# Optimization experiments

Hardware: AMD Instinct MI355X
Metric: run time of the kernel (lower is better)

The kernel has to match this reference:

```python
import jax, jax.numpy as jnp
import numpy as np
from jax import lax

N_SEEDS = 16
N_SAMPS = 32
IN_C = 3
HID = [32, 64, 64]
K = 3
H = W = 64
EPS = 1e-5


def _uniform(key, shape, bound):
    return jax.random.uniform(key, shape, jnp.float32, -bound, bound)


def setup_inputs() -> dict:
    key = jax.random.key(0)
    keys = jax.random.split(key, 32)
    inp = {"x": jax.random.normal(keys[0], (N_SEEDS, N_SAMPS, IN_C, H, W), jnp.float32)}
    c_in = IN_C
    ki = 1
    for li, c_out in enumerate(HID, start=1):
        fan_in = c_in * K * K
        # kaiming_uniform with a=sqrt(5): gain=sqrt(2/(1+5))=sqrt(1/3); bound=sqrt(3)*gain/sqrt(fan)=1/sqrt(fan)
        wb = 1.0 / np.sqrt(fan_in)
        inp[f"w{li}"] = _uniform(keys[ki], (N_SEEDS * c_out, c_in, K, K), wb); ki += 1
        inp[f"b{li}"] = _uniform(keys[ki], (N_SEEDS * c_out,), wb); ki += 1
        inp[f"g{li}"] = jnp.ones((N_SEEDS * c_out,), jnp.float32)
        inp[f"be{li}"] = jnp.zeros((N_SEEDS * c_out,), jnp.float32)
        c_in = c_out
    return inp


def _layer(h, w, b, g, be):
    # grouped conv: groups = N_SEEDS, OIHW weights, NCHW data, stride 1, pad 1
    h = lax.conv_general_dilated(
        h, w, window_strides=(1, 1), padding=((1, 1), (1, 1)),
        feature_group_count=N_SEEDS,
        dimension_numbers=("NCHW", "OIHW", "NCHW"))
    h = h + b[None, :, None, None]
    # BatchNorm2d, training mode: batch statistics over (N, H, W), biased variance
    mean = jnp.mean(h, axis=(0, 2, 3))
    var = jnp.var(h, axis=(0, 2, 3))
    h = (h - mean[None, :, None, None]) * (g / jnp.sqrt(var + EPS))[None, :, None, None] + be[None, :, None, None]
    return jax.nn.relu(h)


def reference(x, w1, b1, g1, be1, w2, b2, g2, be2, w3, b3, g3, be3):
    S, N, C, Hh, Ww = x.shape  # (n_seeds, n_samps, C, H, W)
    h = jnp.swapaxes(x, 0, 1).reshape(N, S * C, Hh, Ww)
    h = _layer(h, w1, b1, g1, be1)
    h = _layer(h, w2, b2, g2, be2)
    h = _layer(h, w3, b3, g3, be3)
    c_out = HID[-1]
    h = h.reshape(N, S, c_out, Hh, Ww)
    return jnp.swapaxes(h, 0, 1)  # (n_seeds, n_samps, C_out, H, W)
```

## Files before the change

### kernel.cpp

```cpp
#include <hip/hip_runtime.h>
#include <cstddef>
#include <cstdint>

typedef __attribute__((ext_vector_type(8))) _Float16 half8;
typedef __attribute__((ext_vector_type(4))) float f32x4;
typedef _Float16 half_t;

#define NS 16
#define NN 32
#define NPIX 4096

static const size_t OFF_H1 = 0;
static const size_t OFF_H2 = 134217728ull;
static const size_t OFF_WT1 = OFF_H2 + 268435456ull;
static const size_t OFF_WT2 = OFF_WT1 + 55296ull;
static const size_t OFF_WT3 = OFF_WT2 + 589824ull;
static const size_t OFF_SUMS = OFF_WT3 + 1179648ull;
static const size_t OFF_PRM = OFF_SUMS + 20480ull;

__global__ __launch_bounds__(256) void transform_k(
    const float* __restrict__ w1, const float* __restrict__ w2,
    const float* __restrict__ w3, float* __restrict__ wt1,
    half_t* __restrict__ wt2, half_t* __restrict__ wt3)
{
    int idx = blockIdx.x * 256 + threadIdx.x;
    if (idx < 13824) {
        int o = idx & 31, tap = (idx >> 5) % 9, ic = (idx / 288) % 3, s = idx / 864;
        wt1[idx] = w1[((s * 32 + o) * 3 + ic) * 9 + tap];
    } else if (idx < 13824 + 294912) {
        int t = idx - 13824;
        int ic = t & 31, oc = (t >> 5) & 63, tap = (t >> 11) % 9, s = t / 18432;
        wt2[t] = (half_t)w2[((s * 64 + oc) * 32 + ic) * 9 + tap];
    } else {
        int t = idx - (13824 + 294912);
        int ic = t & 63, oc = (t >> 6) & 63, tap = (t >> 12) % 9, s = t / 36864;
        wt3[t] = (half_t)w3[((s * 64 + oc) * 64 + ic) * 9 + tap];
    }
}

__global__ __launch_bounds__(256) void conv1_k(
    const float* __restrict__ x, const float* __restrict__ wt1,
    const float* __restrict__ b1, half_t* __restrict__ h1,
    float* __restrict__ sums1)
{
    __shared__ float smem[8512];
    float* xt = smem;
    float* bounce = smem;
    float* statsl = smem + 8448;
    const int tile = blockIdx.x, s = blockIdx.y, n = blockIdx.z;
    const int tx = tile & 3, ty = tile >> 2, tid = threadIdx.x;

    for (int i = tid; i < 972; i += 256) {
        int ic = i / 324, rem = i - ic * 324;
        int py = rem / 18, px = rem - py * 18;
        int gy = ty * 16 + py - 1, gx = tx * 16 + px - 1;
        float v = 0.f;
        if ((unsigned)gy < 64u && (unsigned)gx < 64u)
            v = x[(size_t)(((s * NN + n) * 3 + ic) * 64 + gy) * 64 + gx];
        xt[i] = v;
    }
    if (tid < 64) statsl[tid] = 0.f;
    __syncthreads();

    const int px = tid & 15, py = tid >> 4;
    float acc[32];
#pragma unroll
    for (int o = 0; o < 32; ++o) acc[o] = 0.f;
#pragma unroll
    for (int ic = 0; ic < 3; ++ic)
#pragma unroll
        for (int ky = 0; ky < 3; ++ky)
#pragma unroll
            for (int kx = 0; kx < 3; ++kx) {
                float v = xt[ic * 324 + (py + ky) * 18 + px + kx];
                const float* wp = wt1 + ((s * 3 + ic) * 9 + ky * 3 + kx) * 32;
#pragma unroll
                for (int o = 0; o < 32; ++o) acc[o] = fmaf(wp[o], v, acc[o]);
            }
    const float* bp = b1 + s * 32;
#pragma unroll
    for (int o = 0; o < 32; ++o) acc[o] += bp[o];

    const int gp = (ty * 16 + py) * 64 + tx * 16 + px;
    half8* dst = (half8*)(h1 + ((size_t)((n * NS + s) * NPIX + gp)) * 32);
#pragma unroll
    for (int k = 0; k < 4; ++k) {
        half8 v8;
#pragma unroll
        for (int j = 0; j < 8; ++j) v8[j] = (half_t)acc[k * 8 + j];
        dst[k] = v8;
    }
    __syncthreads();
#pragma unroll
    for (int o = 0; o < 32; ++o) bounce[tid * 33 + o] = acc[o];
    __syncthreads();
    {
        const int oc = tid & 31, grp = tid >> 5;
        float s1 = 0.f, s2 = 0.f;
#pragma unroll 4
        for (int j = 0; j < 32; ++j) {
            float v = bounce[(grp * 32 + j) * 33 + oc];
            s1 += v; s2 += v * v;
        }
        atomicAdd(&statsl[oc * 2], s1);
        atomicAdd(&statsl[oc * 2 + 1], s2);
    }
    __syncthreads();
    if (tid < 64)
        atomicAdd(&sums1[(s * 32 + (tid >> 1)) * 2 + (tid & 1)], statsl[tid]);
}

__global__ void bnparam_k(const float* __restrict__ sums, const float* __restrict__ g,
                          const float* __restrict__ be, float* __restrict__ a,
                          float* __restrict__ b, int C)
{
    int ch = blockIdx.x * 256 + threadIdx.x;
    if (ch >= C) return;
    const float inv = 1.f / 131072.f;
    float mean = sums[ch * 2] * inv;
    float var = sums[ch * 2 + 1] * inv - mean * mean;
    float sc = g[ch] * rsqrtf(var + 1e-5f);
    a[ch] = sc;
    b[ch] = be[ch] - mean * sc;
}

__global__ __launch_bounds__(256) void conv2_k(
    const half_t* __restrict__ h1, const half_t* __restrict__ wt2,
    const float* __restrict__ b2, const float* __restrict__ a1,
    const float* __restrict__ b1p, half_t* __restrict__ h2,
    float* __restrict__ sums2)
{
    __shared__ __align__(16) char smem[33536];
    half_t* out_lds = (half_t*)smem;
    float* pa = (float*)(smem + 32768);
    float* pb = pa + 32;
    float* statsl = (float*)(smem + 33024);

    const int tile = blockIdx.x, s = blockIdx.y, n = blockIdx.z;
    const int tx = tile & 3, ty = tile >> 2, tid = threadIdx.x;

    if (tid < 32) { pa[tid] = a1[s * 32 + tid]; pb[tid] = b1p[s * 32 + tid]; }
    if (tid >= 128) statsl[tid - 128] = 0.f;
    __syncthreads();

    for (int i = tid; i < 1296; i += 256) {
        int p = i >> 2, cc = i & 3;
        int hy = p / 18, hx = p - hy * 18;
        int gy = ty * 16 + hy - 1, gx = tx * 16 + hx - 1;
        half8 v = {};
        if ((unsigned)gy < 64u && (unsigned)gx < 64u) {
            v = *(const half8*)(h1 + ((size_t)((n * NS + s) * NPIX + gy * 64 + gx)) * 32 + cc * 8);
#pragma unroll
            for (int j = 0; j < 8; ++j) {
                float f = fmaf(pa[cc * 8 + j], (float)v[j], pb[cc * 8 + j]);
                v[j] = (half_t)fmaxf(f, 0.f);
            }
        }
        *(half8*)(smem + p * 80 + cc * 16) = v;
    }
    __syncthreads();

    const int l = tid & 63, wv = tid >> 6, l15 = l & 15, g = l >> 4;
    f32x4 acc[4][4];
#pragma unroll
    for (int mt = 0; mt < 4; ++mt)
#pragma unroll
        for (int nt = 0; nt < 4; ++nt) acc[mt][nt] = (f32x4){0.f, 0.f, 0.f, 0.f};

    const half_t* wbase = wt2 + (size_t)(s * 9) * 2048;
#pragma unroll 1
    for (int tap = 0; tap < 9; ++tap) {
        int ky = tap / 3, kx = tap - ky * 3;
        half8 bfrag[4];
#pragma unroll
        for (int nt = 0; nt < 4; ++nt)
            bfrag[nt] = *(const half8*)(wbase + (size_t)tap * 2048 + (nt * 16 + l15) * 32 + g * 8);
#pragma unroll
        for (int mt = 0; mt < 4; ++mt) {
            int p = (wv * 4 + mt + ky) * 18 + l15 + kx;
            half8 afrag = *(const half8*)(smem + p * 80 + g * 16);
#pragma unroll
            for (int nt = 0; nt < 4; ++nt)
                acc[mt][nt] = __builtin_amdgcn_mfma_f32_16x16x32_f16(afrag, bfrag[nt], acc[mt][nt], 0, 0, 0);
        }
    }

    float s1a[4], s2a[4];
#pragma unroll
    for (int nt = 0; nt < 4; ++nt) {
        float bias = b2[s * 64 + nt * 16 + l15];
        float s1 = 0.f, s2 = 0.f;
#pragma unroll
        for (int mt = 0; mt < 4; ++mt)
#pragma unroll
            for (int r = 0; r < 4; ++r) {
                float v = acc[mt][nt][r] + bias;
                acc[mt][nt][r] = v;
                s1 += v; s2 += v * v;
            }
        s1 += __shfl_xor(s1, 16); s1 += __shfl_xor(s1, 32);
        s2 += __shfl_xor(s2, 16); s2 += __shfl_xor(s2, 32);
        s1a[nt] = s1; s2a[nt] = s2;
    }
    if (l < 16) {
#pragma unroll
        for (int nt = 0; nt < 4; ++nt) {
            atomicAdd(&statsl[(nt * 16 + l15) * 2], s1a[nt]);
            atomicAdd(&statsl[(nt * 16 + l15) * 2 + 1], s2a[nt]);
        }
    }
    __syncthreads();

#pragma unroll
    for (int mt = 0; mt < 4; ++mt)
#pragma unroll
        for (int nt = 0; nt < 4; ++nt)
#pragma unroll
            for (int r = 0; r < 4; ++r)
                out_lds[((wv * 4 + mt) * 16 + g * 4 + r) * 64 + nt * 16 + l15] = (half_t)acc[mt][nt][r];
    __syncthreads();

    const size_t base = (size_t)(n * NS + s) * NPIX * 64;
    for (int i = tid; i < 2048; i += 256) {
        int p = i >> 3, cc = i & 7;
        int gp = (ty * 16 + (p >> 4)) * 64 + tx * 16 + (p & 15);
        *(half8*)(h2 + base + (size_t)gp * 64 + cc * 8) = *(half8*)(smem + p * 128 + cc * 16);
    }
    if (tid < 128)
        atomicAdd(&sums2[(s * 64 + (tid >> 1)) * 2 + (tid & 1)], statsl[tid]);
}

__global__ __launch_bounds__(256) void conv3_k(
    const half_t* __restrict__ h2, const half_t* __restrict__ wt3,
    const float* __restrict__ b3, const float* __restrict__ a2,
    const float* __restrict__ b2p, float* __restrict__ out,
    float* __restrict__ sums3)
{
    __shared__ __align__(16) char smem[47680];
    float* pa = (float*)(smem + 46656);
    float* pb = pa + 64;
    float* statsl = (float*)(smem + 47168);

    const int tile = blockIdx.x, s = blockIdx.y, n = blockIdx.z;
    const int tx = tile & 3, ty = tile >> 2, tid = threadIdx.x;

    if (tid < 64) { pa[tid] = a2[s * 64 + tid]; pb[tid] = b2p[s * 64 + tid]; }
    if (tid >= 128) statsl[tid - 128] = 0.f;
    __syncthreads();

    for (int i = tid; i < 2592; i += 256) {
        int p = i >> 3, cc = i & 7;
        int hy = p / 18, hx = p - hy * 18;
        int gy = ty * 16 + hy - 1, gx = tx * 16 + hx - 1;
        half8 v = {};
        if ((unsigned)gy < 64u && (unsigned)gx < 64u) {
            v = *(const half8*)(h2 + ((size_t)((n * NS + s) * NPIX + gy * 64 + gx)) * 64 + cc * 8);
#pragma unroll
            for (int j = 0; j < 8; ++j) {
                float f = fmaf(pa[cc * 8 + j], (float)v[j], pb[cc * 8 + j]);
                v[j] = (half_t)fmaxf(f, 0.f);
            }
        }
        *(half8*)(smem + p * 144 + cc * 16) = v;
    }
    __syncthreads();

    const int l = tid & 63, wv = tid >> 6, l15 = l & 15, g = l >> 4;
    f32x4 acc[4][4];
#pragma unroll
    for (int mt = 0; mt < 4; ++mt)
#pragma unroll
        for (int nt = 0; nt < 4; ++nt) acc[mt][nt] = (f32x4){0.f, 0.f, 0.f, 0.f};

    const half_t* wbase = wt3 + (size_t)(s * 9) * 4096;
#pragma unroll 1
    for (int tap = 0; tap < 9; ++tap) {
        int ky = tap / 3, kx = tap - ky * 3;
        half8 bfrag[4][2];
#pragma unroll
        for (int nt = 0; nt < 4; ++nt)
#pragma unroll
            for (int kc = 0; kc < 2; ++kc)
                bfrag[nt][kc] = *(const half8*)(wbase + (size_t)tap * 4096 + (nt * 16 + l15) * 64 + kc * 32 + g * 8);
#pragma unroll
        for (int mt = 0; mt < 4; ++mt) {
            int p = (wv * 4 + mt + ky) * 18 + l15 + kx;
            half8 af0 = *(const half8*)(smem + p * 144 + g * 16);
            half8 af1 = *(const half8*)(smem + p * 144 + 64 + g * 16);
#pragma unroll
            for (int nt = 0; nt < 4; ++nt) {
                acc[mt][nt] = __builtin_amdgcn_mfma_f32_16x16x32_f16(af0, bfrag[nt][0], acc[mt][nt], 0, 0, 0);
                acc[mt][nt] = __builtin_amdgcn_mfma_f32_16x16x32_f16(af1, bfrag[nt][1], acc[mt][nt], 0, 0, 0);
            }
        }
    }

    float s1a[4], s2a[4];
#pragma unroll
    for (int nt = 0; nt < 4; ++nt) {
        float bias = b3[s * 64 + nt * 16 + l15];
        float s1 = 0.f, s2 = 0.f;
#pragma unroll
        for (int mt = 0; mt < 4; ++mt)
#pragma unroll
            for (int r = 0; r < 4; ++r) {
                float v = acc[mt][nt][r] + bias;
                acc[mt][nt][r] = v;
                s1 += v; s2 += v * v;
            }
        s1 += __shfl_xor(s1, 16); s1 += __shfl_xor(s1, 32);
        s2 += __shfl_xor(s2, 16); s2 += __shfl_xor(s2, 32);
        s1a[nt] = s1; s2a[nt] = s2;
    }
    if (l < 16) {
#pragma unroll
        for (int nt = 0; nt < 4; ++nt) {
            atomicAdd(&statsl[(nt * 16 + l15) * 2], s1a[nt]);
            atomicAdd(&statsl[(nt * 16 + l15) * 2 + 1], s2a[nt]);
        }
    }

#pragma unroll
    for (int mt = 0; mt < 4; ++mt) {
        int gy = ty * 16 + wv * 4 + mt;
#pragma unroll
        for (int nt = 0; nt < 4; ++nt) {
            int c = nt * 16 + l15;
            *(f32x4*)(out + ((size_t)((s * NN + n) * 64 + c) * 64 + gy) * 64 + tx * 16 + g * 4) = acc[mt][nt];
        }
    }
    __syncthreads();
    if (tid < 128)
        atomicAdd(&sums3[(s * 64 + (tid >> 1)) * 2 + (tid & 1)], statsl[tid]);
}

__global__ __launch_bounds__(256) void final_k(float* __restrict__ out,
                                               const float* __restrict__ a3,
                                               const float* __restrict__ b3p)
{
    size_t i = ((size_t)blockIdx.x * 256 + threadIdx.x) * 4;
    int ch = (int)((i >> 12) & 63) + (int)(i >> 23) * 64;
    float sc = a3[ch], sh = b3p[ch];
    f32x4 v = *(f32x4*)(out + i);
#pragma unroll
    for (int r = 0; r < 4; ++r) v[r] = fmaxf(fmaf(sc, v[r], sh), 0.f);
    *(f32x4*)(out + i) = v;
}

extern "C" void kernel_launch(void* const* d_in, const int* in_sizes, int n_in,
                              void* d_out, int out_size, void* d_ws, size_t ws_size,
                              hipStream_t stream)
{
    const float* x   = (const float*)d_in[0];
    const float* w1  = (const float*)d_in[1];
    const float* b1  = (const float*)d_in[2];
    const float* g1  = (const float*)d_in[3];
    const float* be1 = (const float*)d_in[4];
    const float* w2  = (const float*)d_in[5];
    const float* b2  = (const float*)d_in[6];
    const float* g2  = (const float*)d_in[7];
    const float* be2 = (const float*)d_in[8];
    const float* w3  = (const float*)d_in[9];
    const float* b3  = (const float*)d_in[10];
    const float* g3  = (const float*)d_in[11];
    const float* be3 = (const float*)d_in[12];

    char* ws = (char*)d_ws;
    half_t* h1 = (half_t*)(ws + OFF_H1);
    half_t* h2 = (half_t*)(ws + OFF_H2);
    float* wt1 = (float*)(ws + OFF_WT1);
    half_t* wt2 = (half_t*)(ws + OFF_WT2);
    half_t* wt3 = (half_t*)(ws + OFF_WT3);
    float* sums = (float*)(ws + OFF_SUMS);
    float* s1v = sums, *s2v = sums + 1024, *s3v = sums + 3072;
    float* prm = (float*)(ws + OFF_PRM);
    float *a1 = prm, *b1p = prm + 512, *a2 = prm + 1024, *b2p = prm + 2048;
    float *a3 = prm + 3072, *b3p = prm + 4096;
    float* out = (float*)d_out;

    hipMemsetAsync(ws + OFF_SUMS, 0, 20480, stream);
    transform_k<<<3510, 256, 0, stream>>>(w1, w2, w3, wt1, wt2, wt3);
    dim3 grid(16, 16, 32);
    conv1_k<<<grid, 256, 0, stream>>>(x, wt1, b1, h1, s1v);
    bnparam_k<<<2, 256, 0, stream>>>(s1v, g1, be1, a1, b1p, 512);
    conv2_k<<<grid, 256, 0, stream>>>(h1, wt2, b2, a1, b1p, h2, s2v);
    bnparam_k<<<4, 256, 0, stream>>>(s2v, g2, be2, a2, b2p, 1024);
    conv3_k<<<grid, 256, 0, stream>>>(h2, wt3, b3, a2, b2p, out, s3v);
    bnparam_k<<<4, 256, 0, stream>>>(s3v, g3, be3, a3, b3p, 1024);
    final_k<<<131072, 256, 0, stream>>>(out, a3, b3p);
}
```

Before: 962.0 us.

## Fold BN scale into weights, read padded activations directly from global without LDS staging

Folds the previous layer's BatchNorm scale into the next conv's fp16 weights, so the A operand only needs a half-precision add-shift and ReLU, computed as relu(h + b/a)*a. Activations are stored with column padding, and border columns and a shared zero row are filled with values that turn into zero after the shift and ReLU. This lets conv2 and conv3 load MFMA A fragments straight from global memory instead of staging a halo tile in LDS. It removes the LDS fill loop and its barriers and raises the occupancy hints. The costs are redundant global/L2 reads across taps, extra fp16 rounding, and a risk of sign or overflow trouble when a BN scale is negative or tiny.

Result: slower. 1.192 ms (+23.9%).

```diff
diff --git a/kernel.cpp b/kernel.cpp
--- a/kernel.cpp
+++ b/kernel.cpp
@@ -8,39 +8,60 @@
 
 #define NS 16
 #define NN 32
-#define NPIX 4096
-
-static const size_t OFF_H1 = 0;
-static const size_t OFF_H2 = 134217728ull;
-static const size_t OFF_WT1 = OFF_H2 + 268435456ull;
+
+static const size_t OFF_H1P = 0;
+static const size_t OFF_H2P = 138412032ull;
+static const size_t OFF_ZR1 = OFF_H2P + 276824064ull;
+static const size_t OFF_ZR2 = OFF_ZR1 + 67584ull;
+static const size_t OFF_WT1 = OFF_ZR2 + 135168ull;
 static const size_t OFF_WT2 = OFF_WT1 + 55296ull;
 static const size_t OFF_WT3 = OFF_WT2 + 589824ull;
 static const size_t OFF_SUMS = OFF_WT3 + 1179648ull;
 static const size_t OFF_PRM = OFF_SUMS + 20480ull;
-
-__global__ __launch_bounds__(256) void transform_k(
-    const float* __restrict__ w1, const float* __restrict__ w2,
-    const float* __restrict__ w3, float* __restrict__ wt1,
-    half_t* __restrict__ wt2, half_t* __restrict__ wt3)
+static const size_t OFF_TH  = OFF_PRM + 30720ull;
+
+static __device__ __forceinline__ half8 sr8(half8 v, half8 t) {
+    half8 r = v + t;
+    half8 z = {};
+#if defined(__has_builtin) && __has_builtin(__builtin_elementwise_max)
+    return __builtin_elementwise_max(r, z);
+#else
+#pragma unroll
+    for (int j = 0; j < 8; ++j) r[j] = r[j] > (_Float16)0 ? r[j] : (_Float16)0;
+    return r;
+#endif
+}
+
+__global__ __launch_bounds__(256) void transform1_k(
+    const float* __restrict__ w1, float* __restrict__ wt1)
 {
     int idx = blockIdx.x * 256 + threadIdx.x;
-    if (idx < 13824) {
-        int o = idx & 31, tap = (idx >> 5) % 9, ic = (idx / 288) % 3, s = idx / 864;
-        wt1[idx] = w1[((s * 32 + o) * 3 + ic) * 9 + tap];
-    } else if (idx < 13824 + 294912) {
-        int t = idx - 13824;
-        int ic = t & 31, oc = (t >> 5) & 63, tap = (t >> 11) % 9, s = t / 18432;
-        wt2[t] = (half_t)w2[((s * 64 + oc) * 32 + ic) * 9 + tap];
-    } else {
-        int t = idx - (13824 + 294912);
-        int ic = t & 63, oc = (t >> 6) & 63, tap = (t >> 12) % 9, s = t / 36864;
-        wt3[t] = (half_t)w3[((s * 64 + oc) * 64 + ic) * 9 + tap];
-    }
+    if (idx >= 13824) return;
+    int o = idx & 31, tap = (idx >> 5) % 9, ic = (idx / 288) % 3, s = idx / 864;
+    wt1[idx] = w1[((s * 32 + o) * 3 + ic) * 9 + tap];
+}
+
+__global__ __launch_bounds__(256) void wtrans2_k(
+    const float* __restrict__ w2, const float* __restrict__ a1, half_t* __restrict__ wt2)
+{
+    int idx = blockIdx.x * 256 + threadIdx.x;
+    if (idx >= 294912) return;
+    int ic = idx & 31, oc = (idx >> 5) & 63, tap = (idx >> 11) % 9, s = idx / 18432;
+    wt2[idx] = (half_t)(w2[((s * 64 + oc) * 32 + ic) * 9 + tap] * a1[s * 32 + ic]);
+}
+
+__global__ __launch_bounds__(256) void wtrans3_k(
+    const float* __restrict__ w3, const float* __restrict__ a2, half_t* __restrict__ wt3)
+{
+    int idx = blockIdx.x * 256 + threadIdx.x;
+    if (idx >= 589824) return;
+    int ic = idx & 63, oc = (idx >> 6) & 63, tap = (idx >> 12) % 9, s = idx / 36864;
+    wt3[idx] = (half_t)(w3[((s * 64 + oc) * 64 + ic) * 9 + tap] * a2[s * 64 + ic]);
 }
 
 __global__ __launch_bounds__(256) void conv1_k(
     const float* __restrict__ x, const float* __restrict__ wt1,
-    const float* __restrict__ b1, half_t* __restrict__ h1,
+    const float* __restrict__ b1, half_t* __restrict__ h1p,
     float* __restrict__ sums1)
 {
     __shared__ float smem[8512];
@@ -81,8 +102,8 @@
 #pragma unroll
     for (int o = 0; o < 32; ++o) acc[o] += bp[o];
 
-    const int gp = (ty * 16 + py) * 64 + tx * 16 + px;
-    half8* dst = (half8*)(h1 + ((size_t)((n * NS + s) * NPIX + gp)) * 32);
+    const int gy1 = ty * 16 + py, gxp = tx * 16 + px + 1;
+    half8* dst = (half8*)(h1p + (size_t)(n * NS + s) * 135168 + (size_t)(gy1 * 66 + gxp) * 32);
 #pragma unroll
     for (int k = 0; k < 4; ++k) {
         half8 v8;
@@ -112,7 +133,8 @@
 
 __global__ void bnparam_k(const float* __restrict__ sums, const float* __restrict__ g,
                           const float* __restrict__ be, float* __restrict__ a,
-                          float* __restrict__ b, int C)
+                          float* __restrict__ b, float* __restrict__ t,
+                          half_t* __restrict__ th, int C)
 {
     int ch = blockIdx.x * 256 + threadIdx.x;
     if (ch >= C) return;
@@ -121,67 +143,84 @@
     float var = sums[ch * 2 + 1] * inv - mean * mean;
     float sc = g[ch] * rsqrtf(var + 1e-5f);
     a[ch] = sc;
-    b[ch] = be[ch] - mean * sc;
-}
-
-__global__ __launch_bounds__(256) void conv2_k(
-    const half_t* __restrict__ h1, const half_t* __restrict__ wt2,
-    const float* __restrict__ b2, const float* __restrict__ a1,
-    const float* __restrict__ b1p, half_t* __restrict__ h2,
+    float bb = be[ch] - mean * sc;
+    b[ch] = bb;
+    float tt = bb / sc;
+    t[ch] = tt;
+    th[ch] = (half_t)tt;
+}
+
+__global__ __launch_bounds__(256) void padfill_k(
+    half_t* __restrict__ img, half_t* __restrict__ zrow, const float* __restrict__ t,
+    int C, int c8shift, long imgstride, int rowstride, long tot_cols, long tot)
+{
+    long idx = (long)blockIdx.x * 256 + threadIdx.x;
+    if (idx >= tot) return;
+    const int nc8m = (1 << c8shift) - 1;
+    if (idx < tot_cols) {
+        int c8 = (int)idx & nc8m; long r = idx >> c8shift;
+        int side = (int)r & 1; r >>= 1;
+        int y = (int)r & 63; r >>= 6;
+        int si = (int)(r & 15); int ni = (int)(r >> 4);
+        half8 q;
+#pragma unroll
+        for (int j = 0; j < 8; ++j) q[j] = (half_t)(-(t[si * C + c8 * 8 + j] + 1.0f));
+        *(half8*)(img + (long)(ni * NS + si) * imgstride + (long)y * rowstride +
+                  (side ? 65 : 0) * C + c8 * 8) = q;
+    } else {
+        long r2 = idx - tot_cols;
+        int c8 = (int)r2 & nc8m; r2 >>= c8shift;
+        int xx = (int)(r2 % 66); int si = (int)(r2 / 66);
+        half8 q;
+#pragma unroll
+        for (int j = 0; j < 8; ++j) q[j] = (half_t)(-(t[si * C + c8 * 8 + j] + 1.0f));
+        *(half8*)(zrow + ((long)(si * 66 + xx)) * C + c8 * 8) = q;
+    }
+}
+
+__global__ __launch_bounds__(256, 4) void conv2_k(
+    const half_t* __restrict__ h1p, const half_t* __restrict__ zr1,
+    const half_t* __restrict__ wt2, const float* __restrict__ b2,
+    const half_t* __restrict__ th1, half_t* __restrict__ h2p,
     float* __restrict__ sums2)
 {
-    __shared__ __align__(16) char smem[33536];
-    half_t* out_lds = (half_t*)smem;
-    float* pa = (float*)(smem + 32768);
-    float* pb = pa + 32;
-    float* statsl = (float*)(smem + 33024);
-
+    __shared__ __align__(16) half_t obuf[256 * 72];
+    __shared__ float statsl[128];
     const int tile = blockIdx.x, s = blockIdx.y, n = blockIdx.z;
     const int tx = tile & 3, ty = tile >> 2, tid = threadIdx.x;
-
-    if (tid < 32) { pa[tid] = a1[s * 32 + tid]; pb[tid] = b1p[s * 32 + tid]; }
-    if (tid >= 128) statsl[tid - 128] = 0.f;
-    __syncthreads();
-
-    for (int i = tid; i < 1296; i += 256) {
-        int p = i >> 2, cc = i & 3;
-        int hy = p / 18, hx = p - hy * 18;
-        int gy = ty * 16 + hy - 1, gx = tx * 16 + hx - 1;
-        half8 v = {};
-        if ((unsigned)gy < 64u && (unsigned)gx < 64u) {
-            v = *(const half8*)(h1 + ((size_t)((n * NS + s) * NPIX + gy * 64 + gx)) * 32 + cc * 8);
-#pragma unroll
-            for (int j = 0; j < 8; ++j) {
-                float f = fmaf(pa[cc * 8 + j], (float)v[j], pb[cc * 8 + j]);
-                v[j] = (half_t)fmaxf(f, 0.f);
-            }
-        }
-        *(half8*)(smem + p * 80 + cc * 16) = v;
-    }
-    __syncthreads();
-
     const int l = tid & 63, wv = tid >> 6, l15 = l & 15, g = l >> 4;
+    if (tid < 128) statsl[tid] = 0.f;
+    __syncthreads();
+
+    const half_t* img = h1p + (size_t)(n * NS + s) * 135168;
+    const half_t* zrow = zr1 + s * 2112;
+    const half8 tsh = *(const half8*)(th1 + s * 32 + g * 8);
+    const half_t* wb = wt2 + (size_t)s * 18432;
+    const int laneoff = l15 * 32 + g * 8;
+
     f32x4 acc[4][4];
 #pragma unroll
     for (int mt = 0; mt < 4; ++mt)
 #pragma unroll
         for (int nt = 0; nt < 4; ++nt) acc[mt][nt] = (f32x4){0.f, 0.f, 0.f, 0.f};
 
-    const half_t* wbase = wt2 + (size_t)(s * 9) * 2048;
 #pragma unroll 1
     for (int tap = 0; tap < 9; ++tap) {
-        int ky = tap / 3, kx = tap - ky * 3;
-        half8 bfrag[4];
+        const int ky = tap / 3, kx = tap - ky * 3;
+        half8 bf[4];
 #pragma unroll
         for (int nt = 0; nt < 4; ++nt)
-            bfrag[nt] = *(const half8*)(wbase + (size_t)tap * 2048 + (nt * 16 + l15) * 32 + g * 8);
+            bf[nt] = *(const half8*)(wb + (tap * 64 + nt * 16 + l15) * 32 + g * 8);
+        const int xb = (tx * 16 + kx) * 32;
 #pragma unroll
         for (int mt = 0; mt < 4; ++mt) {
-            int p = (wv * 4 + mt + ky) * 18 + l15 + kx;
-            half8 afrag = *(const half8*)(smem + p * 80 + g * 16);
+            const int gy = ty * 16 + wv * 4 + mt + ky - 1;
+            const half_t* rp = zrow;
+            if ((unsigned)gy < 64u) rp = img + gy * 2112;
+            half8 av = sr8(*(const half8*)(rp + xb + laneoff), tsh);
 #pragma unroll
             for (int nt = 0; nt < 4; ++nt)
-                acc[mt][nt] = __builtin_amdgcn_mfma_f32_16x16x32_f16(afrag, bfrag[nt], acc[mt][nt], 0, 0, 0);
+                acc[mt][nt] = __builtin_amdgcn_mfma_f32_16x16x32_f16(av, bf[nt], acc[mt][nt], 0, 0, 0);
         }
     }
 
@@ -209,7 +248,6 @@
             atomicAdd(&statsl[(nt * 16 + l15) * 2 + 1], s2a[nt]);
         }
     }
-    __syncthreads();
 
 #pragma unroll
     for (int mt = 0; mt < 4; ++mt)
@@ -217,80 +255,66 @@
         for (int nt = 0; nt < 4; ++nt)
 #pragma unroll
             for (int r = 0; r < 4; ++r)
-                out_lds[((wv * 4 + mt) * 16 + g * 4 + r) * 64 + nt * 16 + l15] = (half_t)acc[mt][nt][r];
-    __syncthreads();
-
-    const size_t base = (size_t)(n * NS + s) * NPIX * 64;
+                obuf[((wv * 4 + mt) * 16 + g * 4 + r) * 72 + nt * 16 + l15] = (half_t)acc[mt][nt][r];
+    __syncthreads();
+
+    half_t* img2 = h2p + (size_t)(n * NS + s) * 270336;
     for (int i = tid; i < 2048; i += 256) {
         int p = i >> 3, cc = i & 7;
-        int gp = (ty * 16 + (p >> 4)) * 64 + tx * 16 + (p & 15);
-        *(half8*)(h2 + base + (size_t)gp * 64 + cc * 8) = *(half8*)(smem + p * 128 + cc * 16);
+        int y = ty * 16 + (p >> 4), xp = tx * 16 + (p & 15) + 1;
+        *(half8*)(img2 + (size_t)y * 4224 + xp * 64 + cc * 8) = *(const half8*)(obuf + p * 72 + cc * 8);
     }
     if (tid < 128)
         atomicAdd(&sums2[(s * 64 + (tid >> 1)) * 2 + (tid & 1)], statsl[tid]);
 }
 
-__global__ __launch_bounds__(256) void conv3_k(
-    const half_t* __restrict__ h2, const half_t* __restrict__ wt3,
-    const float* __restrict__ b3, const float* __restrict__ a2,
-    const float* __restrict__ b2p, float* __restrict__ out,
+__global__ __launch_bounds__(256, 3) void conv3_k(
+    const half_t* __restrict__ h2p, const half_t* __restrict__ zr2,
+    const half_t* __restrict__ wt3, const float* __restrict__ b3,
+    const half_t* __restrict__ th2, float* __restrict__ out,
     float* __restrict__ sums3)
 {
-    __shared__ __align__(16) char smem[47680];
-    float* pa = (float*)(smem + 46656);
-    float* pb = pa + 64;
-    float* statsl = (float*)(smem + 47168);
-
+    __shared__ float statsl[128];
     const int tile = blockIdx.x, s = blockIdx.y, n = blockIdx.z;
     const int tx = tile & 3, ty = tile >> 2, tid = threadIdx.x;
-
-    if (tid < 64) { pa[tid] = a2[s * 64 + tid]; pb[tid] = b2p[s * 64 + tid]; }
-    if (tid >= 128) statsl[tid - 128] = 0.f;
-    __syncthreads();
-
-    for (int i = tid; i < 2592; i += 256) {
-        int p = i >> 3, cc = i & 7;
-        int hy = p / 18, hx = p - hy * 18;
-        int gy = ty * 16 + hy - 1, gx = tx * 16 + hx - 1;
-        half8 v = {};
-        if ((unsigned)gy < 64u && (unsigned)gx < 64u) {
-            v = *(const half8*)(h2 + ((size_t)((n * NS + s) * NPIX + gy * 64 + gx)) * 64 + cc * 8);
-#pragma unroll
-            for (int j = 0; j < 8; ++j) {
-                float f = fmaf(pa[cc * 8 + j], (float)v[j], pb[cc * 8 + j]);
-                v[j] = (half_t)fmaxf(f, 0.f);
-            }
-        }
-        *(half8*)(smem + p * 144 + cc * 16) = v;
-    }
-    __syncthreads();
-
     const int l = tid & 63, wv = tid >> 6, l15 = l & 15, g = l >> 4;
+    if (tid < 128) statsl[tid] = 0.f;
+    __syncthreads();
+
+    const half_t* img = h2p + (size_t)(n * NS + s) * 270336;
+    const half_t* zrow = zr2 + s * 4224;
+    const half8 tsh0 = *(const half8*)(th2 + s * 64 + g * 8);
+    const half8 tsh1 = *(const half8*)(th2 + s * 64 + 32 + g * 8);
+    const half_t* wb = wt3 + (size_t)s * 36864;
+    const int laneoff = l15 * 64 + g * 8;
+
     f32x4 acc[4][4];
 #pragma unroll
     for (int mt = 0; mt < 4; ++mt)
 #pragma unroll
         for (int nt = 0; nt < 4; ++nt) acc[mt][nt] = (f32x4){0.f, 0.f, 0.f, 0.f};
 
-    const half_t* wbase = wt3 + (size_t)(s * 9) * 4096;
 #pragma unroll 1
     for (int tap = 0; tap < 9; ++tap) {
-        int ky = tap / 3, kx = tap - ky * 3;
-        half8 bfrag[4][2];
-#pragma unroll
-        for (int nt = 0; nt < 4; ++nt)
-#pragma unroll
-            for (int kc = 0; kc < 2; ++kc)
-                bfrag[nt][kc] = *(const half8*)(wbase + (size_t)tap * 4096 + (nt * 16 + l15) * 64 + kc * 32 + g * 8);
+        const int ky = tap / 3, kx = tap - ky * 3;
+        half8 bf0[4], bf1[4];
+#pragma unroll
+        for (int nt = 0; nt < 4; ++nt) {
+            bf0[nt] = *(const half8*)(wb + (tap * 64 + nt * 16 + l15) * 64 + g * 8);
+            bf1[nt] = *(const half8*)(wb + (tap * 64 + nt * 16 + l15) * 64 + 32 + g * 8);
+        }
+        const int xb = (tx * 16 + kx) * 64;
 #pragma unroll
         for (int mt = 0; mt < 4; ++mt) {
-            int p = (wv * 4 + mt + ky) * 18 + l15 + kx;
-            half8 af0 = *(const half8*)(smem + p * 144 + g * 16);
-            half8 af1 = *(const half8*)(smem + p * 144 + 64 + g * 16);
+            const int gy = ty * 16 + wv * 4 + mt + ky - 1;
+            const half_t* rp = zrow;
+            if ((unsigned)gy < 64u) rp = img + gy * 4224;
+            half8 a0 = sr8(*(const half8*)(rp + xb + laneoff), tsh0);
+            half8 a1 = sr8(*(const half8*)(rp + xb + laneoff + 32), tsh1);
 #pragma unroll
             for (int nt = 0; nt < 4; ++nt) {
-                acc[mt][nt] = __builtin_amdgcn_mfma_f32_16x16x32_f16(af0, bfrag[nt][0], acc[mt][nt], 0, 0, 0);
-                acc[mt][nt] = __builtin_amdgcn_mfma_f32_16x16x32_f16(af1, bfrag[nt][1], acc[mt][nt], 0, 0, 0);
+                acc[mt][nt] = __builtin_amdgcn_mfma_f32_16x16x32_f16(a0, bf0[nt], acc[mt][nt], 0, 0, 0);
+                acc[mt][nt] = __builtin_amdgcn_mfma_f32_16x16x32_f16(a1, bf1[nt], acc[mt][nt], 0, 0, 0);
             }
         }
     }
@@ -366,26 +390,35 @@
     const float* be3 = (const float*)d_in[12];
 
     char* ws = (char*)d_ws;
-    half_t* h1 = (half_t*)(ws + OFF_H1);
-    half_t* h2 = (half_t*)(ws + OFF_H2);
-    float* wt1 = (float*)(ws + OFF_WT1);
+    half_t* h1p = (half_t*)(ws + OFF_H1P);
+    half_t* h2p = (half_t*)(ws + OFF_H2P);
+    half_t* zr1 = (half_t*)(ws + OFF_ZR1);
+    half_t* zr2 = (half_t*)(ws + OFF_ZR2);
+    float*  wt1 = (float*)(ws + OFF_WT1);
     half_t* wt2 = (half_t*)(ws + OFF_WT2);
     half_t* wt3 = (half_t*)(ws + OFF_WT3);
-    float* sums = (float*)(ws + OFF_SUMS);
-    float* s1v = sums, *s2v = sums + 1024, *s3v = sums + 3072;
-    float* prm = (float*)(ws + OFF_PRM);
-    float *a1 = prm, *b1p = prm + 512, *a2 = prm + 1024, *b2p = prm + 2048;
-    float *a3 = prm + 3072, *b3p = prm + 4096;
+    float*  sums = (float*)(ws + OFF_SUMS);
+    float *s1v = sums, *s2v = sums + 1024, *s3v = sums + 3072;
+    float*  prm = (float*)(ws + OFF_PRM);
+    float *a1 = prm,        *b1p = prm + 512,  *t1 = prm + 1024;
+    float *a2 = prm + 1536, *b2p = prm + 2560, *t2 = prm + 3584;
+    float *a3 = prm + 4608, *b3p = prm + 5632, *t3 = prm + 6656;
+    half_t* th = (half_t*)(ws + OFF_TH);
+    half_t *th1 = th, *th2 = th + 512, *th3 = th + 1536;
     float* out = (float*)d_out;
 
     hipMemsetAsync(ws + OFF_SUMS, 0, 20480, stream);
-    transform_k<<<3510, 256, 0, stream>>>(w1, w2, w3, wt1, wt2, wt3);
+    transform1_k<<<54, 256, 0, stream>>>(w1, wt1);
     dim3 grid(16, 16, 32);
-    conv1_k<<<grid, 256, 0, stream>>>(x, wt1, b1, h1, s1v);
-    bnparam_k<<<2, 256, 0, stream>>>(s1v, g1, be1, a1, b1p, 512);
-    conv2_k<<<grid, 256, 0, stream>>>(h1, wt2, b2, a1, b1p, h2, s2v);
-    bnparam_k<<<4, 256, 0, stream>>>(s2v, g2, be2, a2, b2p, 1024);
-    conv3_k<<<grid, 256, 0, stream>>>(h2, wt3, b3, a2, b2p, out, s3v);
-    bnparam_k<<<4, 256, 0, stream>>>(s3v, g3, be3, a3, b3p, 1024);
+    conv1_k<<<grid, 256, 0, stream>>>(x, wt1, b1, h1p, s1v);
+    bnparam_k<<<2, 256, 0, stream>>>(s1v, g1, be1, a1, b1p, t1, th1, 512);
+    padfill_k<<<1041, 256, 0, stream>>>(h1p, zr1, t1, 32, 2, 135168L, 2112, 262144L, 266368L);
+    wtrans2_k<<<1152, 256, 0, stream>>>(w2, a1, wt2);
+    conv2_k<<<grid, 256, 0, stream>>>(h1p, zr1, wt2, b2, th1, h2p, s2v);
+    bnparam_k<<<4, 256, 0, stream>>>(s2v, g2, be2, a2, b2p, t2, th2, 1024);
+    padfill_k<<<2081, 256, 0, stream>>>(h2p, zr2, t2, 64, 3, 270336L, 4224, 524288L, 532736L);
+    wtrans3_k<<<2304, 256, 0, stream>>>(w3, a2, wt3);
+    conv3_k<<<grid, 256, 0, stream>>>(h2p, zr2, wt3, b3, th2, out, s3v);
+    bnparam_k<<<4, 256, 0, stream>>>(s3v, g3, be3, a3, b3p, t3, th3, 1024);
     final_k<<<131072, 256, 0, stream>>>(out, a3, b3p);
 }
```
